# Kernel optimization log

Measured on AMD Instinct MI355X. Metric: run time of the kernel, lower is better.

The kernel has to match this reference:

```python
import jax, jax.numpy as jnp
import numpy as np

T, N, F, H, C, E = 8, 50000, 128, 64, 4, 800000


def setup_inputs() -> dict:
    key = jax.random.key(0)
    ks = jax.random.split(key, 8)
    x = jax.random.normal(ks[0], (T, N, F), jnp.float32)
    edges = jax.random.randint(ks[1], (T, 2, E), 0, N, jnp.int32)
    # GCNConv weights (one per timestep, glorot-ish scale) + Linear layers
    Wg = jax.random.normal(ks[2], (T, F, H), jnp.float32) / np.sqrt(F)
    bg = jnp.zeros((T, H), jnp.float32)
    W1 = jax.random.normal(ks[3], (H, 32), jnp.float32) / np.sqrt(H)
    b1 = jnp.zeros((32,), jnp.float32)
    W2 = jax.random.normal(ks[4], (32, 16), jnp.float32) / np.sqrt(32)
    b2 = jnp.zeros((16,), jnp.float32)
    W3 = jax.random.normal(ks[5], (16, C), jnp.float32) / np.sqrt(16)
    b3 = jnp.zeros((C,), jnp.float32)
    return dict(x=x, edges=edges, Wg=Wg, bg=bg, W1=W1, b1=b1, W2=W2, b2=b2, W3=W3, b3=b3)


def gcn_conv(x, edge_index, W, b):
    """PyG GCNConv: add self-loops, sym-normalized aggregation of x @ W, plus bias."""
    n = x.shape[0]
    loop = jnp.arange(n, dtype=edge_index.dtype)
    src = jnp.concatenate([edge_index[0], loop])  # message sources
    dst = jnp.concatenate([edge_index[1], loop])  # aggregation targets
    deg = jax.ops.segment_sum(jnp.ones_like(dst, dtype=x.dtype), dst, num_segments=n)
    dinv = jnp.where(deg > 0, jax.lax.rsqrt(deg), 0.0)
    xw = x @ W                                    # [n, H]
    norm = (dinv[src] * dinv[dst])[:, None]       # [E+n, 1]
    out = jax.ops.segment_sum(xw[src] * norm, dst, num_segments=n)
    return out + b


def reference(x, edges, Wg, bg, W1, b1, W2, b2, W3, b3):
    def step(acc, inp):
        xt, et, Wt, bt = inp
        return acc + jax.nn.relu(gcn_conv(xt, et, Wt, bt)), None

    acc0 = jnp.zeros((x.shape[1], Wg.shape[-1]), x.dtype)
    h, _ = jax.lax.scan(step, acc0, (x, edges, Wg, bg))  # sum over T timesteps
    h = jax.nn.relu(h)                 # dropout omitted (eval mode)
    h = jax.nn.relu(h @ W1 + b1)
    h = jax.nn.relu(h @ W2 + b2)
    logits = h @ W3 + b3
    return jax.nn.log_softmax(logits, axis=1)
```

## Files before the change

kernel.cpp:

```cpp
#include <hip/hip_runtime.h>
#include <hip/hip_bf16.h>

#define TT 8
#define NN 50000
#define FF 128
#define HH 64
#define CC 4
#define EE 800000
#define NB2 391
#define CAP 2560
#define BPT 125

typedef unsigned short u16;
typedef unsigned int u32;
typedef __attribute__((ext_vector_type(8))) short bf16x8;
typedef __attribute__((ext_vector_type(4))) float f32x4;
typedef __attribute__((ext_vector_type(4))) int i32x4;

static __device__ __forceinline__ float bflo(u32 w) {
    union { unsigned int i; float f; } v; v.i = w << 16; return v.f;
}
static __device__ __forceinline__ float bfhi(u32 w) {
    union { unsigned int i; float f; } v; v.i = w & 0xFFFF0000u; return v.f;
}
static __device__ __forceinline__ u16 cvt_bf16(float f) {
    __hip_bfloat16 b = __float2bfloat16(f);
    return *reinterpret_cast<u16*>(&b);
}

__global__ __launch_bounds__(256) void zero_gcur_kernel(int* __restrict__ gcur) {
    int i = blockIdx.x * 256 + threadIdx.x;
    if (i < TT * NB2) gcur[i] = 0;
}

__global__ __launch_bounds__(256) void multisplit_kernel(const int* __restrict__ edges,
                                                         int* __restrict__ gcur, u32* __restrict__ binned) {
    __shared__ u32 sbuf[NB2][16];
    __shared__ int scnt[NB2];
    int bid = blockIdx.x;
    int t = bid & 7;
    int blk = bid >> 3;
    const int per = EE / BPT;
    int e0 = blk * per;
    int e1 = e0 + per;

    for (int i = threadIdx.x; i < NB2; i += 256) scnt[i] = 0;
    __syncthreads();

    const int* es = edges + (size_t)(t * 2 + 0) * EE;
    const int* ed = edges + (size_t)(t * 2 + 1) * EE;
    int* gc = gcur + t * NB2;
    u32* bb = binned + (size_t)t * NB2 * CAP;

    for (int base = e0; base < e1; base += 1024) {
        u32 rec[4]; int pb[4];
        int e = base + threadIdx.x * 4;
        int nv = 0;
        if (e + 3 < e1) nv = 4;
        else if (e < e1) nv = e1 - e;
        if (nv == 4) {
            i32x4 s4 = *reinterpret_cast<const i32x4*>(&es[e]);
            i32x4 d4 = *reinterpret_cast<const i32x4*>(&ed[e]);
            #pragma unroll
            for (int q = 0; q < 4; ++q) {
                int b = d4[q] >> 7;
                u32 r = (u32)s4[q] | ((u32)(d4[q] & 127) << 16);
                int p = atomicAdd(&scnt[b], 1);
                if (p < 16) { sbuf[b][p] = r; pb[q] = -1; }
                else { rec[q] = r; pb[q] = b; }
            }
        } else {
            #pragma unroll
            for (int q = 0; q < 4; ++q) {
                pb[q] = -1;
                if (q < nv) {
                    int src = es[e + q], dst = ed[e + q];
                    int b = dst >> 7;
                    u32 r = (u32)src | ((u32)(dst & 127) << 16);
                    int p = atomicAdd(&scnt[b], 1);
                    if (p < 16) sbuf[b][p] = r;
                    else { rec[q] = r; pb[q] = b; }
                }
            }
        }
        __syncthreads();
        for (int fb = threadIdx.x; fb < NB2; fb += 256) {
            if (scnt[fb] >= 16) {
                int g = atomicAdd(&gc[fb], 16);
                uint4* dp = (uint4*)(bb + (size_t)fb * CAP + g);
                uint4* sp = (uint4*)&sbuf[fb][0];
                dp[0] = sp[0]; dp[1] = sp[1]; dp[2] = sp[2]; dp[3] = sp[3];
                scnt[fb] = 0;
            }
        }
        __syncthreads();
        #pragma unroll
        for (int q = 0; q < 4; ++q) {
            if (pb[q] >= 0) {
                int p = atomicAdd(&scnt[pb[q]], 1);
                if (p < 16) sbuf[pb[q]][p] = rec[q];
                else { int g = atomicAdd(&gc[pb[q]], 1); bb[(size_t)pb[q] * CAP + g] = rec[q]; }
            }
        }
        __syncthreads();
    }
    for (int fb = threadIdx.x; fb < NB2; fb += 256) {
        int c = scnt[fb];
        if (c > 0) {
            int g = atomicAdd(&gc[fb], c);
            for (int k = 0; k < c; ++k) bb[(size_t)fb * CAP + g + k] = sbuf[fb][k];
        }
    }
}

__global__ __launch_bounds__(512) void csr_scatter_kernel(const u32* __restrict__ binned, const int* __restrict__ gcur,
                                                          u16* __restrict__ srclist, u32* __restrict__ nodeinfo,
                                                          float* __restrict__ dinv) {
    __shared__ u32 recs[CAP];
    __shared__ int hist[128];
    __shared__ int cur[128];
    int b = blockIdx.x, t = blockIdx.y, tid = threadIdx.x;
    int node0 = b * 128;
    int tot = gcur[t * NB2 + b];
    const u32* win = binned + ((size_t)t * NB2 + b) * CAP;

    for (int i = tid; i < tot; i += 512) recs[i] = win[i];
    if (tid < 128) hist[tid] = 0;
    __syncthreads();
    for (int i = tid; i < tot; i += 512) atomicAdd(&hist[recs[i] >> 16], 1);
    __syncthreads();
    if (tid < 64) {
        int v0 = hist[2 * tid], v1 = hist[2 * tid + 1];
        int pair = v0 + v1;
        int inc = pair;
        #pragma unroll
        for (int off = 1; off < 64; off <<= 1) {
            int u = __shfl_up(inc, off, 64);
            if (tid >= off) inc += u;
        }
        int exclp = inc - pair;
        cur[2 * tid] = exclp;
        cur[2 * tid + 1] = exclp + v0;
        int node = node0 + 2 * tid;
        if (node < NN) {
            nodeinfo[t * NN + node] = (u32)(b * CAP + exclp) | ((u32)v0 << 20);
            dinv[t * NN + node] = rsqrtf(1.0f + (float)v0);
        }
        if (node + 1 < NN) {
            nodeinfo[t * NN + node + 1] = (u32)(b * CAP + exclp + v0) | ((u32)v1 << 20);
            dinv[t * NN + node + 1] = rsqrtf(1.0f + (float)v1);
        }
    }
    __syncthreads();
    u16* sl = srclist + (size_t)t * NB2 * CAP;
    for (int i = tid; i < tot; i += 512) {
        u32 rec = recs[i];
        int d = rec >> 16;
        int p = atomicAdd(&cur[d], 1);
        sl[(size_t)b * CAP + p] = (u16)(rec & 0xFFFF);
    }
}

__global__ __launch_bounds__(256) void wt_prep_kernel(const float* __restrict__ Wg, u16* __restrict__ wt) {
    int t = blockIdx.x;
    const float* w = Wg + t * FF * HH;
    u16* o = wt + (size_t)t * HH * FF;
    for (int i = threadIdx.x; i < FF * HH; i += 256) {
        int k = i >> 6, c = i & 63;
        o[c * FF + k] = cvt_bf16(w[i]);
    }
}

__global__ __launch_bounds__(512) void xw_kernel(const float* __restrict__ x, const u16* __restrict__ wt,
                                                 const float* __restrict__ dinv, u16* __restrict__ y) {
    int t = blockIdx.y;
    int row0 = blockIdx.x * 256;
    int tid = threadIdx.x;
    int w = tid >> 6, lane = tid & 63;
    int l15 = lane & 15, lg = lane >> 4;
    __shared__ __align__(16) u16 ylds[256][72];
    const float* xt = x + (size_t)t * NN * FF;
    const u16* wtt = wt + (size_t)t * HH * FF;

    f32x4 d[2][4] = {{{0,0,0,0},{0,0,0,0},{0,0,0,0},{0,0,0,0}},
                     {{0,0,0,0},{0,0,0,0},{0,0,0,0},{0,0,0,0}}};
    #pragma unroll
    for (int k0 = 0; k0 < 128; k0 += 32) {
        int kb = k0 + lg * 8;
        union { bf16x8 v; __hip_bfloat162 h[4]; } au[2];
        #pragma unroll
        for (int s = 0; s < 2; ++s) {
            int arow = row0 + w * 32 + s * 16 + l15;
            if (arow < NN) {
                f32x4 f0 = __builtin_nontemporal_load(reinterpret_cast<const f32x4*>(&xt[(size_t)arow * FF + kb]));
                f32x4 f1 = __builtin_nontemporal_load(reinterpret_cast<const f32x4*>(&xt[(size_t)arow * FF + kb + 4]));
                au[s].h[0] = __float22bfloat162_rn(make_float2(f0[0], f0[1]));
                au[s].h[1] = __float22bfloat162_rn(make_float2(f0[2], f0[3]));
                au[s].h[2] = __float22bfloat162_rn(make_float2(f1[0], f1[1]));
                au[s].h[3] = __float22bfloat162_rn(make_float2(f1[2], f1[3]));
            } else {
                au[s].v = (bf16x8){0,0,0,0,0,0,0,0};
            }
        }
        #pragma unroll
        for (int n = 0; n < 4; ++n) {
            bf16x8 bf = *reinterpret_cast<const bf16x8*>(&wtt[(size_t)(n * 16 + l15) * FF + kb]);
            d[0][n] = __builtin_amdgcn_mfma_f32_16x16x32_bf16(au[0].v, bf, d[0][n], 0, 0, 0);
            d[1][n] = __builtin_amdgcn_mfma_f32_16x16x32_bf16(au[1].v, bf, d[1][n], 0, 0, 0);
        }
    }
    #pragma unroll
    for (int s = 0; s < 2; ++s) {
        int rl = w * 32 + s * 16 + lg * 4;
        float dv[4];
        #pragma unroll
        for (int i = 0; i < 4; ++i) {
            int grow = row0 + rl + i;
            dv[i] = (grow < NN) ? dinv[t * NN + grow] : 0.f;
        }
        #pragma unroll
        for (int n = 0; n < 4; ++n) {
            int col = n * 16 + l15;
            #pragma unroll
            for (int i = 0; i < 4; ++i)
                ylds[rl + i][col] = cvt_bf16(d[s][n][i] * dv[i]);
        }
    }
    __syncthreads();
    u16* yt = y + (size_t)t * NN * HH;
    #pragma unroll
    for (int it = 0; it < 4; ++it) {
        int idx = it * 512 + tid;
        int r = idx >> 3, c8 = (idx & 7) * 8;
        int grow = row0 + r;
        if (grow < NN)
            *reinterpret_cast<uint4*>(&yt[(size_t)grow * HH + c8]) =
                *reinterpret_cast<const uint4*>(&ylds[r][c8]);
    }
}

__global__ __launch_bounds__(256) void agg_kernel(const u16* __restrict__ y, const float* __restrict__ dinv,
                                                  const u32* __restrict__ nodeinfo, const u16* __restrict__ srclist,
                                                  const float* __restrict__ bg, float* __restrict__ acc) {
    int node = blockIdx.x * 4 + (threadIdx.x >> 6);
    int lane = threadIdx.x & 63;
    int sub = lane >> 4;
    int fo = lane & 15;
    float a0 = 0.f, a1 = 0.f, a2 = 0.f, a3 = 0.f;
    for (int t = 0; t < TT; ++t) {
        const u16* yt = y + (size_t)t * NN * HH;
        u32 info = nodeinfo[t * NN + node];
        int cnt = info >> 20;
        const u16* sl = srclist + (size_t)t * NB2 * CAP + (info & 0xFFFFF);
        float s0 = 0.f, s1 = 0.f, s2 = 0.f, s3 = 0.f;
        int j = 0;
        for (; j + 16 <= cnt; j += 16) {
            int e0 = sl[j + sub], e1 = sl[j + 4 + sub], e2 = sl[j + 8 + sub], e3 = sl[j + 12 + sub];
            uint2 v0 = *reinterpret_cast<const uint2*>(&yt[(size_t)e0 * HH + fo * 4]);
            uint2 v1 = *reinterpret_cast<const uint2*>(&yt[(size_t)e1 * HH + fo * 4]);
            uint2 v2 = *reinterpret_cast<const uint2*>(&yt[(size_t)e2 * HH + fo * 4]);
            uint2 v3 = *reinterpret_cast<const uint2*>(&yt[(size_t)e3 * HH + fo * 4]);
            s0 += (bflo(v0.x) + bflo(v1.x)) + (bflo(v2.x) + bflo(v3.x));
            s1 += (bfhi(v0.x) + bfhi(v1.x)) + (bfhi(v2.x) + bfhi(v3.x));
            s2 += (bflo(v0.y) + bflo(v1.y)) + (bflo(v2.y) + bflo(v3.y));
            s3 += (bfhi(v0.y) + bfhi(v1.y)) + (bfhi(v2.y) + bfhi(v3.y));
        }
        for (; j < cnt; j += 4) {
            int e = j + sub;
            uint2 v = make_uint2(0u, 0u);
            if (e < cnt) {
                int srcid = sl[e];
                v = *reinterpret_cast<const uint2*>(&yt[(size_t)srcid * HH + fo * 4]);
            }
            s0 += bflo(v.x);
            s1 += bfhi(v.x);
            s2 += bflo(v.y);
            s3 += bfhi(v.y);
        }
        s0 += __shfl_xor(s0, 16, 64); s0 += __shfl_xor(s0, 32, 64);
        s1 += __shfl_xor(s1, 16, 64); s1 += __shfl_xor(s1, 32, 64);
        s2 += __shfl_xor(s2, 16, 64); s2 += __shfl_xor(s2, 32, 64);
        s3 += __shfl_xor(s3, 16, 64); s3 += __shfl_xor(s3, 32, 64);
        uint2 sv = *reinterpret_cast<const uint2*>(&yt[(size_t)node * HH + fo * 4]);
        s0 += bflo(sv.x);
        s1 += bfhi(sv.x);
        s2 += bflo(sv.y);
        s3 += bfhi(sv.y);
        float dvv = dinv[t * NN + node];
        float4 bgv = *reinterpret_cast<const float4*>(&bg[t * HH + fo * 4]);
        a0 += fmaxf(dvv * s0 + bgv.x, 0.f);
        a1 += fmaxf(dvv * s1 + bgv.y, 0.f);
        a2 += fmaxf(dvv * s2 + bgv.z, 0.f);
        a3 += fmaxf(dvv * s3 + bgv.w, 0.f);
    }
    if (sub == 0) {
        float4 o = make_float4(a0, a1, a2, a3);
        *reinterpret_cast<float4*>(&acc[(size_t)node * HH + fo * 4]) = o;
    }
}

__global__ __launch_bounds__(256) void head_kernel(const float* __restrict__ acc,
                                                   const float* __restrict__ W1, const float* __restrict__ b1,
                                                   const float* __restrict__ W2, const float* __restrict__ b2,
                                                   const float* __restrict__ W3, const float* __restrict__ b3,
                                                   float* __restrict__ out) {
    __shared__ float w1[64 * 32], w2[32 * 16], w3[16 * 4], bb1[32], bb2[16], bb3[4];
    int tid = threadIdx.x;
    for (int i = tid; i < 2048; i += 256) w1[i] = W1[i];
    for (int i = tid; i < 512; i += 256) w2[i] = W2[i];
    if (tid < 64) w3[tid] = W3[tid];
    if (tid < 32) bb1[tid] = b1[tid];
    if (tid < 16) bb2[tid] = b2[tid];
    if (tid < 4) bb3[tid] = b3[tid];
    __syncthreads();
    int node = blockIdx.x * 256 + tid;
    if (node >= NN) return;

    float a[64];
    #pragma unroll
    for (int k = 0; k < 64; ++k) a[k] = acc[(size_t)node * HH + k];

    float h1[32];
    for (int j = 0; j < 32; ++j) {
        float s = bb1[j];
        #pragma unroll
        for (int k = 0; k < 64; ++k) s += a[k] * w1[k * 32 + j];
        h1[j] = fmaxf(s, 0.f);
    }
    float h2[16];
    for (int j = 0; j < 16; ++j) {
        float s = bb2[j];
        #pragma unroll
        for (int k = 0; k < 32; ++k) s += h1[k] * w2[k * 16 + j];
        h2[j] = fmaxf(s, 0.f);
    }
    float l[4];
    for (int c = 0; c < 4; ++c) {
        float s = bb3[c];
        #pragma unroll
        for (int k = 0; k < 16; ++k) s += h2[k] * w3[k * 4 + c];
        l[c] = s;
    }
    float m = fmaxf(fmaxf(l[0], l[1]), fmaxf(l[2], l[3]));
    float sum = 0.f;
    #pragma unroll
    for (int c = 0; c < 4; ++c) sum += expf(l[c] - m);
    float lse = logf(sum);
    float4 o;
    o.x = l[0] - m - lse; o.y = l[1] - m - lse; o.z = l[2] - m - lse; o.w = l[3] - m - lse;
    *reinterpret_cast<float4*>(&out[(size_t)node * CC]) = o;
}

extern "C" void kernel_launch(void* const* d_in, const int* in_sizes, int n_in,
                              void* d_out, int out_size, void* d_ws, size_t ws_size,
                              hipStream_t stream) {
    const float* x    = (const float*)d_in[0];
    const int*  edges = (const int*)d_in[1];
    const float* Wg   = (const float*)d_in[2];
    const float* bg   = (const float*)d_in[3];
    const float* W1   = (const float*)d_in[4];
    const float* b1   = (const float*)d_in[5];
    const float* W2   = (const float*)d_in[6];
    const float* b2   = (const float*)d_in[7];
    const float* W3   = (const float*)d_in[8];
    const float* b3   = (const float*)d_in[9];
    float* out = (float*)d_out;

    char* ws = (char*)d_ws;
    size_t o = 0;
    int* gcur      = (int*)(ws + o); o += (size_t)TT * NB2 * 4;
    o = (o + 255) & ~(size_t)255;
    float* dinv    = (float*)(ws + o); o += (size_t)TT * NN * 4;
    u32* nodeinfo  = (u32*)(ws + o); o += (size_t)TT * NN * 4;
    o = (o + 255) & ~(size_t)255;
    u16* wt        = (u16*)(ws + o); o += (size_t)TT * HH * FF * 2;
    o = (o + 255) & ~(size_t)255;
    u32* binned    = (u32*)(ws + o); o += (size_t)TT * NB2 * CAP * 4;
    u16* srclist   = (u16*)(ws + o); o += (size_t)TT * NB2 * CAP * 2;
    u16* y         = (u16*)(ws + o); o += (size_t)TT * NN * HH * 2;
    float* acc     = (float*)(ws + o); o += (size_t)NN * HH * 4;

    zero_gcur_kernel<<<(TT * NB2 + 255) / 256, 256, 0, stream>>>(gcur);

    multisplit_kernel<<<BPT * TT, 256, 0, stream>>>(edges, gcur, binned);

    dim3 gsc(NB2, TT);
    csr_scatter_kernel<<<gsc, 512, 0, stream>>>(binned, gcur, srclist, nodeinfo, dinv);

    wt_prep_kernel<<<TT, 256, 0, stream>>>(Wg, wt);

    dim3 gx(196, TT);
    xw_kernel<<<gx, 512, 0, stream>>>(x, wt, dinv, y);

    agg_kernel<<<12500, 256, 0, stream>>>(y, dinv, nodeinfo, srclist, bg, acc);

    head_kernel<<<196, 256, 0, stream>>>(acc, W1, b1, W2, b2, W3, b3, out);
}
```

Before: 338.3 us.

## Count degrees in multisplit and co-schedule CSR build with XW GEMM

Per-node in-degree is now counted with global atomics during the edge multisplit pass. This lets the CSR scatter and the x@W GEMM run as interleaved block roles of a single launch, instead of the GEMM waiting on a separate CSR kernel for dinv. The dinv array is dropped: each consumer recomputes it from the degree counts with rsqrt. The aggregation loop is also unrolled to 32 edges per iteration to keep more gathers in flight. In exchange, it adds 6.4M global atomics on a zeroed 1.6MB count array and a larger zeroing kernel.

```diff
diff --git a/kernel.cpp b/kernel.cpp
--- a/kernel.cpp
+++ b/kernel.cpp
@@ -10,6 +10,7 @@
 #define NB2 391
 #define CAP 2560
 #define BPT 125
+#define XWB 196
 
 typedef unsigned short u16;
 typedef unsigned int u32;
@@ -28,13 +29,15 @@
     return *reinterpret_cast<u16*>(&b);
 }
 
-__global__ __launch_bounds__(256) void zero_gcur_kernel(int* __restrict__ gcur) {
+__global__ __launch_bounds__(256) void zero_kernel(int* __restrict__ cnt, int* __restrict__ gcur) {
     int i = blockIdx.x * 256 + threadIdx.x;
-    if (i < TT * NB2) gcur[i] = 0;
+    if (i < TT * NN) cnt[i] = 0;
+    else if (i < TT * NN + TT * NB2) gcur[i - TT * NN] = 0;
 }
 
 __global__ __launch_bounds__(256) void multisplit_kernel(const int* __restrict__ edges,
-                                                         int* __restrict__ gcur, u32* __restrict__ binned) {
+                                                         int* __restrict__ gcur, u32* __restrict__ binned,
+                                                         int* __restrict__ cnt) {
     __shared__ u32 sbuf[NB2][16];
     __shared__ int scnt[NB2];
     int bid = blockIdx.x;
@@ -50,6 +53,7 @@
     const int* es = edges + (size_t)(t * 2 + 0) * EE;
     const int* ed = edges + (size_t)(t * 2 + 1) * EE;
     int* gc = gcur + t * NB2;
+    int* cw = cnt + t * NN;
     u32* bb = binned + (size_t)t * NB2 * CAP;
 
     for (int base = e0; base < e1; base += 1024) {
@@ -65,6 +69,7 @@
             for (int q = 0; q < 4; ++q) {
                 int b = d4[q] >> 7;
                 u32 r = (u32)s4[q] | ((u32)(d4[q] & 127) << 16);
+                atomicAdd(&cw[d4[q]], 1);
                 int p = atomicAdd(&scnt[b], 1);
                 if (p < 16) { sbuf[b][p] = r; pb[q] = -1; }
                 else { rec[q] = r; pb[q] = b; }
@@ -77,6 +82,7 @@
                     int src = es[e + q], dst = ed[e + q];
                     int b = dst >> 7;
                     u32 r = (u32)src | ((u32)(dst & 127) << 16);
+                    atomicAdd(&cw[dst], 1);
                     int p = atomicAdd(&scnt[b], 1);
                     if (p < 16) sbuf[b][p] = r;
                     else { rec[q] = r; pb[q] = b; }
@@ -113,54 +119,6 @@
     }
 }
 
-__global__ __launch_bounds__(512) void csr_scatter_kernel(const u32* __restrict__ binned, const int* __restrict__ gcur,
-                                                          u16* __restrict__ srclist, u32* __restrict__ nodeinfo,
-                                                          float* __restrict__ dinv) {
-    __shared__ u32 recs[CAP];
-    __shared__ int hist[128];
-    __shared__ int cur[128];
-    int b = blockIdx.x, t = blockIdx.y, tid = threadIdx.x;
-    int node0 = b * 128;
-    int tot = gcur[t * NB2 + b];
-    const u32* win = binned + ((size_t)t * NB2 + b) * CAP;
-
-    for (int i = tid; i < tot; i += 512) recs[i] = win[i];
-    if (tid < 128) hist[tid] = 0;
-    __syncthreads();
-    for (int i = tid; i < tot; i += 512) atomicAdd(&hist[recs[i] >> 16], 1);
-    __syncthreads();
-    if (tid < 64) {
-        int v0 = hist[2 * tid], v1 = hist[2 * tid + 1];
-        int pair = v0 + v1;
-        int inc = pair;
-        #pragma unroll
-        for (int off = 1; off < 64; off <<= 1) {
-            int u = __shfl_up(inc, off, 64);
-            if (tid >= off) inc += u;
-        }
-        int exclp = inc - pair;
-        cur[2 * tid] = exclp;
-        cur[2 * tid + 1] = exclp + v0;
-        int node = node0 + 2 * tid;
-        if (node < NN) {
-            nodeinfo[t * NN + node] = (u32)(b * CAP + exclp) | ((u32)v0 << 20);
-            dinv[t * NN + node] = rsqrtf(1.0f + (float)v0);
-        }
-        if (node + 1 < NN) {
-            nodeinfo[t * NN + node + 1] = (u32)(b * CAP + exclp + v0) | ((u32)v1 << 20);
-            dinv[t * NN + node + 1] = rsqrtf(1.0f + (float)v1);
-        }
-    }
-    __syncthreads();
-    u16* sl = srclist + (size_t)t * NB2 * CAP;
-    for (int i = tid; i < tot; i += 512) {
-        u32 rec = recs[i];
-        int d = rec >> 16;
-        int p = atomicAdd(&cur[d], 1);
-        sl[(size_t)b * CAP + p] = (u16)(rec & 0xFFFF);
-    }
-}
-
 __global__ __launch_bounds__(256) void wt_prep_kernel(const float* __restrict__ Wg, u16* __restrict__ wt) {
     int t = blockIdx.x;
     const float* w = Wg + t * FF * HH;
@@ -171,75 +129,124 @@
     }
 }
 
-__global__ __launch_bounds__(512) void xw_kernel(const float* __restrict__ x, const u16* __restrict__ wt,
-                                                 const float* __restrict__ dinv, u16* __restrict__ y) {
-    int t = blockIdx.y;
-    int row0 = blockIdx.x * 256;
+__global__ __launch_bounds__(512) void build_kernel(const u32* __restrict__ binned, const int* __restrict__ gcur,
+                                                    const int* __restrict__ cnt,
+                                                    u16* __restrict__ srclist, u32* __restrict__ nodeinfo,
+                                                    const float* __restrict__ x, const u16* __restrict__ wt,
+                                                    u16* __restrict__ y) {
+    __shared__ __align__(16) char smem[256 * 72 * 2];
+    int bid = blockIdx.x;
     int tid = threadIdx.x;
-    int w = tid >> 6, lane = tid & 63;
-    int l15 = lane & 15, lg = lane >> 4;
-    __shared__ __align__(16) u16 ylds[256][72];
-    const float* xt = x + (size_t)t * NN * FF;
-    const u16* wtt = wt + (size_t)t * HH * FF;
-
-    f32x4 d[2][4] = {{{0,0,0,0},{0,0,0,0},{0,0,0,0},{0,0,0,0}},
-                     {{0,0,0,0},{0,0,0,0},{0,0,0,0},{0,0,0,0}}};
-    #pragma unroll
-    for (int k0 = 0; k0 < 128; k0 += 32) {
-        int kb = k0 + lg * 8;
-        union { bf16x8 v; __hip_bfloat162 h[4]; } au[2];
+    int isXw, id;
+    if (bid < 2 * XWB * TT) { isXw = ((bid & 1) == 0); id = bid >> 1; }
+    else { isXw = 0; id = XWB * TT + (bid - 2 * XWB * TT); }
+
+    if (!isXw) {
+        u32* recs = (u32*)smem;
+        int* cur = (int*)(smem + CAP * 4);
+        int t = id / NB2, b = id % NB2;
+        int node0 = b * 128;
+        int tot = gcur[t * NB2 + b];
+        const u32* win = binned + ((size_t)t * NB2 + b) * CAP;
+        const int* cw = cnt + t * NN;
+        for (int i = tid; i < tot; i += 512) recs[i] = win[i];
+        __syncthreads();
+        if (tid < 64) {
+            int n0 = node0 + 2 * tid;
+            int v0 = (n0 < NN) ? cw[n0] : 0;
+            int v1 = (n0 + 1 < NN) ? cw[n0 + 1] : 0;
+            int pair = v0 + v1;
+            int inc = pair;
+            #pragma unroll
+            for (int off = 1; off < 64; off <<= 1) {
+                int u = __shfl_up(inc, off, 64);
+                if (tid >= off) inc += u;
+            }
+            int exclp = inc - pair;
+            cur[2 * tid] = exclp;
+            cur[2 * tid + 1] = exclp + v0;
+            if (n0 < NN)
+                nodeinfo[t * NN + n0] = (u32)(b * CAP + exclp) | ((u32)v0 << 20);
+            if (n0 + 1 < NN)
+                nodeinfo[t * NN + n0 + 1] = (u32)(b * CAP + exclp + v0) | ((u32)v1 << 20);
+        }
+        __syncthreads();
+        u16* sl = srclist + (size_t)t * NB2 * CAP;
+        for (int i = tid; i < tot; i += 512) {
+            u32 rec = recs[i];
+            int d = rec >> 16;
+            int p = atomicAdd(&cur[d], 1);
+            sl[(size_t)b * CAP + p] = (u16)(rec & 0xFFFF);
+        }
+    } else {
+        u16 (*ylds)[72] = (u16(*)[72])smem;
+        int t = id / XWB, xb = id % XWB;
+        int row0 = xb * 256;
+        int w = tid >> 6, lane = tid & 63;
+        int l15 = lane & 15, lg = lane >> 4;
+        const float* xt = x + (size_t)t * NN * FF;
+        const u16* wtt = wt + (size_t)t * HH * FF;
+        const int* cw = cnt + t * NN;
+
+        f32x4 d[2][4] = {{{0,0,0,0},{0,0,0,0},{0,0,0,0},{0,0,0,0}},
+                         {{0,0,0,0},{0,0,0,0},{0,0,0,0},{0,0,0,0}}};
+        #pragma unroll
+        for (int k0 = 0; k0 < 128; k0 += 32) {
+            int kb = k0 + lg * 8;
+            union { bf16x8 v; __hip_bfloat162 h[4]; } au[2];
+            #pragma unroll
+            for (int s = 0; s < 2; ++s) {
+                int arow = row0 + w * 32 + s * 16 + l15;
+                if (arow < NN) {
+                    f32x4 f0 = __builtin_nontemporal_load(reinterpret_cast<const f32x4*>(&xt[(size_t)arow * FF + kb]));
+                    f32x4 f1 = __builtin_nontemporal_load(reinterpret_cast<const f32x4*>(&xt[(size_t)arow * FF + kb + 4]));
+                    au[s].h[0] = __float22bfloat162_rn(make_float2(f0[0], f0[1]));
+                    au[s].h[1] = __float22bfloat162_rn(make_float2(f0[2], f0[3]));
+                    au[s].h[2] = __float22bfloat162_rn(make_float2(f1[0], f1[1]));
+                    au[s].h[3] = __float22bfloat162_rn(make_float2(f1[2], f1[3]));
+                } else {
+                    au[s].v = (bf16x8){0,0,0,0,0,0,0,0};
+                }
+            }
+            #pragma unroll
+            for (int n = 0; n < 4; ++n) {
+                bf16x8 bf = *reinterpret_cast<const bf16x8*>(&wtt[(size_t)(n * 16 + l15) * FF + kb]);
+                d[0][n] = __builtin_amdgcn_mfma_f32_16x16x32_bf16(au[0].v, bf, d[0][n], 0, 0, 0);
+                d[1][n] = __builtin_amdgcn_mfma_f32_16x16x32_bf16(au[1].v, bf, d[1][n], 0, 0, 0);
+            }
+        }
         #pragma unroll
         for (int s = 0; s < 2; ++s) {
-            int arow = row0 + w * 32 + s * 16 + l15;
-            if (arow < NN) {
-                f32x4 f0 = __builtin_nontemporal_load(reinterpret_cast<const f32x4*>(&xt[(size_t)arow * FF + kb]));
-                f32x4 f1 = __builtin_nontemporal_load(reinterpret_cast<const f32x4*>(&xt[(size_t)arow * FF + kb + 4]));
-                au[s].h[0] = __float22bfloat162_rn(make_float2(f0[0], f0[1]));
-                au[s].h[1] = __float22bfloat162_rn(make_float2(f0[2], f0[3]));
-                au[s].h[2] = __float22bfloat162_rn(make_float2(f1[0], f1[1]));
-                au[s].h[3] = __float22bfloat162_rn(make_float2(f1[2], f1[3]));
-            } else {
-                au[s].v = (bf16x8){0,0,0,0,0,0,0,0};
-            }
-        }
-        #pragma unroll
-        for (int n = 0; n < 4; ++n) {
-            bf16x8 bf = *reinterpret_cast<const bf16x8*>(&wtt[(size_t)(n * 16 + l15) * FF + kb]);
-            d[0][n] = __builtin_amdgcn_mfma_f32_16x16x32_bf16(au[0].v, bf, d[0][n], 0, 0, 0);
-            d[1][n] = __builtin_amdgcn_mfma_f32_16x16x32_bf16(au[1].v, bf, d[1][n], 0, 0, 0);
-        }
-    }
-    #pragma unroll
-    for (int s = 0; s < 2; ++s) {
-        int rl = w * 32 + s * 16 + lg * 4;
-        float dv[4];
-        #pragma unroll
-        for (int i = 0; i < 4; ++i) {
-            int grow = row0 + rl + i;
-            dv[i] = (grow < NN) ? dinv[t * NN + grow] : 0.f;
-        }
-        #pragma unroll
-        for (int n = 0; n < 4; ++n) {
-            int col = n * 16 + l15;
-            #pragma unroll
-            for (int i = 0; i < 4; ++i)
-                ylds[rl + i][col] = cvt_bf16(d[s][n][i] * dv[i]);
-        }
-    }
-    __syncthreads();
-    u16* yt = y + (size_t)t * NN * HH;
-    #pragma unroll
-    for (int it = 0; it < 4; ++it) {
-        int idx = it * 512 + tid;
-        int r = idx >> 3, c8 = (idx & 7) * 8;
-        int grow = row0 + r;
-        if (grow < NN)
-            *reinterpret_cast<uint4*>(&yt[(size_t)grow * HH + c8]) =
-                *reinterpret_cast<const uint4*>(&ylds[r][c8]);
-    }
-}
-
-__global__ __launch_bounds__(256) void agg_kernel(const u16* __restrict__ y, const float* __restrict__ dinv,
+            int rl = w * 32 + s * 16 + lg * 4;
+            float dv[4];
+            #pragma unroll
+            for (int i = 0; i < 4; ++i) {
+                int grow = row0 + rl + i;
+                dv[i] = (grow < NN) ? rsqrtf(1.f + (float)cw[grow]) : 0.f;
+            }
+            #pragma unroll
+            for (int n = 0; n < 4; ++n) {
+                int col = n * 16 + l15;
+                #pragma unroll
+                for (int i = 0; i < 4; ++i)
+                    ylds[rl + i][col] = cvt_bf16(d[s][n][i] * dv[i]);
+            }
+        }
+        __syncthreads();
+        u16* yt = y + (size_t)t * NN * HH;
+        #pragma unroll
+        for (int it = 0; it < 4; ++it) {
+            int idx = it * 512 + tid;
+            int r = idx >> 3, c8 = (idx & 7) * 8;
+            int grow = row0 + r;
+            if (grow < NN)
+                *reinterpret_cast<uint4*>(&yt[(size_t)grow * HH + c8]) =
+                    *reinterpret_cast<const uint4*>(&ylds[r][c8]);
+        }
+    }
+}
+
+__global__ __launch_bounds__(256) void agg_kernel(const u16* __restrict__ y,
                                                   const u32* __restrict__ nodeinfo, const u16* __restrict__ srclist,
                                                   const float* __restrict__ bg, float* __restrict__ acc) {
     int node = blockIdx.x * 4 + (threadIdx.x >> 6);
@@ -254,7 +261,27 @@
         const u16* sl = srclist + (size_t)t * NB2 * CAP + (info & 0xFFFFF);
         float s0 = 0.f, s1 = 0.f, s2 = 0.f, s3 = 0.f;
         int j = 0;
-        for (; j + 16 <= cnt; j += 16) {
+        for (; j + 32 <= cnt; j += 32) {
+            int e0 = sl[j + sub],      e1 = sl[j + 4 + sub],  e2 = sl[j + 8 + sub],  e3 = sl[j + 12 + sub];
+            int e4 = sl[j + 16 + sub], e5 = sl[j + 20 + sub], e6 = sl[j + 24 + sub], e7 = sl[j + 28 + sub];
+            uint2 v0 = *reinterpret_cast<const uint2*>(&yt[(size_t)e0 * HH + fo * 4]);
+            uint2 v1 = *reinterpret_cast<const uint2*>(&yt[(size_t)e1 * HH + fo * 4]);
+            uint2 v2 = *reinterpret_cast<const uint2*>(&yt[(size_t)e2 * HH + fo * 4]);
+            uint2 v3 = *reinterpret_cast<const uint2*>(&yt[(size_t)e3 * HH + fo * 4]);
+            uint2 v4 = *reinterpret_cast<const uint2*>(&yt[(size_t)e4 * HH + fo * 4]);
+            uint2 v5 = *reinterpret_cast<const uint2*>(&yt[(size_t)e5 * HH + fo * 4]);
+            uint2 v6 = *reinterpret_cast<const uint2*>(&yt[(size_t)e6 * HH + fo * 4]);
+            uint2 v7 = *reinterpret_cast<const uint2*>(&yt[(size_t)e7 * HH + fo * 4]);
+            s0 += ((bflo(v0.x) + bflo(v1.x)) + (bflo(v2.x) + bflo(v3.x)))
+                + ((bflo(v4.x) + bflo(v5.x)) + (bflo(v6.x) + bflo(v7.x)));
+            s1 += ((bfhi(v0.x) + bfhi(v1.x)) + (bfhi(v2.x) + bfhi(v3.x)))
+                + ((bfhi(v4.x) + bfhi(v5.x)) + (bfhi(v6.x) + bfhi(v7.x)));
+            s2 += ((bflo(v0.y) + bflo(v1.y)) + (bflo(v2.y) + bflo(v3.y)))
+                + ((bflo(v4.y) + bflo(v5.y)) + (bflo(v6.y) + bflo(v7.y)));
+            s3 += ((bfhi(v0.y) + bfhi(v1.y)) + (bfhi(v2.y) + bfhi(v3.y)))
+                + ((bfhi(v4.y) + bfhi(v5.y)) + (bfhi(v6.y) + bfhi(v7.y)));
+        }
+        if (j + 16 <= cnt) {
             int e0 = sl[j + sub], e1 = sl[j + 4 + sub], e2 = sl[j + 8 + sub], e3 = sl[j + 12 + sub];
             uint2 v0 = *reinterpret_cast<const uint2*>(&yt[(size_t)e0 * HH + fo * 4]);
             uint2 v1 = *reinterpret_cast<const uint2*>(&yt[(size_t)e1 * HH + fo * 4]);
@@ -264,6 +291,7 @@
             s1 += (bfhi(v0.x) + bfhi(v1.x)) + (bfhi(v2.x) + bfhi(v3.x));
             s2 += (bflo(v0.y) + bflo(v1.y)) + (bflo(v2.y) + bflo(v3.y));
             s3 += (bfhi(v0.y) + bfhi(v1.y)) + (bfhi(v2.y) + bfhi(v3.y));
+            j += 16;
         }
         for (; j < cnt; j += 4) {
             int e = j + sub;
@@ -286,7 +314,7 @@
         s1 += bfhi(sv.x);
         s2 += bflo(sv.y);
         s3 += bfhi(sv.y);
-        float dvv = dinv[t * NN + node];
+        float dvv = rsqrtf(1.f + (float)cnt);
         float4 bgv = *reinterpret_cast<const float4*>(&bg[t * HH + fo * 4]);
         a0 += fmaxf(dvv * s0 + bgv.x, 0.f);
         a1 += fmaxf(dvv * s1 + bgv.y, 0.f);
@@ -370,7 +398,7 @@
     size_t o = 0;
     int* gcur      = (int*)(ws + o); o += (size_t)TT * NB2 * 4;
     o = (o + 255) & ~(size_t)255;
-    float* dinv    = (float*)(ws + o); o += (size_t)TT * NN * 4;
+    int* cnt       = (int*)(ws + o); o += (size_t)TT * NN * 4;
     u32* nodeinfo  = (u32*)(ws + o); o += (size_t)TT * NN * 4;
     o = (o + 255) & ~(size_t)255;
     u16* wt        = (u16*)(ws + o); o += (size_t)TT * HH * FF * 2;
@@ -380,19 +408,16 @@
     u16* y         = (u16*)(ws + o); o += (size_t)TT * NN * HH * 2;
     float* acc     = (float*)(ws + o); o += (size_t)NN * HH * 4;
 
-    zero_gcur_kernel<<<(TT * NB2 + 255) / 256, 256, 0, stream>>>(gcur);
-
-    multisplit_kernel<<<BPT * TT, 256, 0, stream>>>(edges, gcur, binned);
-
-    dim3 gsc(NB2, TT);
-    csr_scatter_kernel<<<gsc, 512, 0, stream>>>(binned, gcur, srclist, nodeinfo, dinv);
+    zero_kernel<<<(TT * NN + TT * NB2 + 255) / 256, 256, 0, stream>>>(cnt, gcur);
 
     wt_prep_kernel<<<TT, 256, 0, stream>>>(Wg, wt);
 
-    dim3 gx(196, TT);
-    xw_kernel<<<gx, 512, 0, stream>>>(x, wt, dinv, y);
-
-    agg_kernel<<<12500, 256, 0, stream>>>(y, dinv, nodeinfo, srclist, bg, acc);
+    multisplit_kernel<<<BPT * TT, 256, 0, stream>>>(edges, gcur, binned, cnt);
+
+    build_kernel<<<XWB * TT + NB2 * TT, 512, 0, stream>>>(binned, gcur, cnt, srclist, nodeinfo,
+                                                          x, wt, y);
+
+    agg_kernel<<<12500, 256, 0, stream>>>(y, nodeinfo, srclist, bg, acc);
 
     head_kernel<<<196, 256, 0, stream>>>(acc, W1, b1, W2, b2, W3, b3, out);
 }
```

After: 583.7 us. 72.5% more time.

## Merge edge multisplit and XW GEMM into one interleaved kernel

Applied to the files above, without the earlier changes.

Fuses the edge-binning multisplit and the dense X·W bf16 MFMA GEMM into a single launch whose blocks are interleaved, one multisplit block per three GEMM blocks, so the atomic-heavy binning overlaps the bandwidth-bound GEMM. The dinv source scaling moves out of the GEMM epilogue into csr_scatter, which rescales y in place per bucket. The dinv buffer goes away because agg recomputes rsqrt from the count. The cost is an extra read-modify-write pass over y, a second bf16 rounding of y, and GEMM blocks shrunk to 128 rows and 256 threads.

```diff
diff --git a/kernel.cpp b/kernel.cpp
--- a/kernel.cpp
+++ b/kernel.cpp
@@ -10,6 +10,7 @@
 #define NB2 391
 #define CAP 2560
 #define BPT 125
+#define XWB 391
 
 typedef unsigned short u16;
 typedef unsigned int u32;
@@ -33,89 +34,171 @@
     if (i < TT * NB2) gcur[i] = 0;
 }
 
-__global__ __launch_bounds__(256) void multisplit_kernel(const int* __restrict__ edges,
-                                                         int* __restrict__ gcur, u32* __restrict__ binned) {
-    __shared__ u32 sbuf[NB2][16];
-    __shared__ int scnt[NB2];
+__global__ __launch_bounds__(256) void wt_prep_kernel(const float* __restrict__ Wg, u16* __restrict__ wt) {
+    int t = blockIdx.x;
+    const float* w = Wg + t * FF * HH;
+    u16* o = wt + (size_t)t * HH * FF;
+    for (int i = threadIdx.x; i < FF * HH; i += 256) {
+        int k = i >> 6, c = i & 63;
+        o[c * FF + k] = cvt_bf16(w[i]);
+    }
+}
+
+__global__ __launch_bounds__(256) void ms_xw_kernel(const int* __restrict__ edges,
+                                                    int* __restrict__ gcur, u32* __restrict__ binned,
+                                                    const float* __restrict__ x, const u16* __restrict__ wt,
+                                                    u16* __restrict__ y) {
+    __shared__ __align__(16) char smem[26624];
     int bid = blockIdx.x;
-    int t = bid & 7;
-    int blk = bid >> 3;
-    const int per = EE / BPT;
-    int e0 = blk * per;
-    int e1 = e0 + per;
-
-    for (int i = threadIdx.x; i < NB2; i += 256) scnt[i] = 0;
-    __syncthreads();
-
-    const int* es = edges + (size_t)(t * 2 + 0) * EE;
-    const int* ed = edges + (size_t)(t * 2 + 1) * EE;
-    int* gc = gcur + t * NB2;
-    u32* bb = binned + (size_t)t * NB2 * CAP;
-
-    for (int base = e0; base < e1; base += 1024) {
-        u32 rec[4]; int pb[4];
-        int e = base + threadIdx.x * 4;
-        int nv = 0;
-        if (e + 3 < e1) nv = 4;
-        else if (e < e1) nv = e1 - e;
-        if (nv == 4) {
-            i32x4 s4 = *reinterpret_cast<const i32x4*>(&es[e]);
-            i32x4 d4 = *reinterpret_cast<const i32x4*>(&ed[e]);
+    int tid = threadIdx.x;
+    int isMs, id;
+    if (bid < 4 * BPT * TT) {
+        isMs = ((bid & 3) == 0);
+        id = isMs ? (bid >> 2) : ((bid >> 2) * 3 + (bid & 3) - 1);
+    } else {
+        isMs = 0; id = 3 * BPT * TT + (bid - 4 * BPT * TT);
+    }
+
+    if (isMs) {
+        u32 (*sbuf)[16] = (u32(*)[16])smem;
+        int* scnt = (int*)(smem + NB2 * 16 * 4);
+        int t = id & 7;
+        int blk = id >> 3;
+        const int per = EE / BPT;
+        int e0 = blk * per;
+        int e1 = e0 + per;
+
+        for (int i = tid; i < NB2; i += 256) scnt[i] = 0;
+        __syncthreads();
+
+        const int* es = edges + (size_t)(t * 2 + 0) * EE;
+        const int* ed = edges + (size_t)(t * 2 + 1) * EE;
+        int* gc = gcur + t * NB2;
+        u32* bb = binned + (size_t)t * NB2 * CAP;
+
+        for (int base = e0; base < e1; base += 1024) {
+            u32 rec[4]; int pb[4];
+            int e = base + tid * 4;
+            int nv = 0;
+            if (e + 3 < e1) nv = 4;
+            else if (e < e1) nv = e1 - e;
+            if (nv == 4) {
+                i32x4 s4 = *reinterpret_cast<const i32x4*>(&es[e]);
+                i32x4 d4 = *reinterpret_cast<const i32x4*>(&ed[e]);
+                #pragma unroll
+                for (int q = 0; q < 4; ++q) {
+                    int b = d4[q] >> 7;
+                    u32 r = (u32)s4[q] | ((u32)(d4[q] & 127) << 16);
+                    int p = atomicAdd(&scnt[b], 1);
+                    if (p < 16) { sbuf[b][p] = r; pb[q] = -1; }
+                    else { rec[q] = r; pb[q] = b; }
+                }
+            } else {
+                #pragma unroll
+                for (int q = 0; q < 4; ++q) {
+                    pb[q] = -1;
+                    if (q < nv) {
+                        int src = es[e + q], dst = ed[e + q];
+                        int b = dst >> 7;
+                        u32 r = (u32)src | ((u32)(dst & 127) << 16);
+                        int p = atomicAdd(&scnt[b], 1);
+                        if (p < 16) sbuf[b][p] = r;
+                        else { rec[q] = r; pb[q] = b; }
+                    }
+                }
+            }
+            __syncthreads();
+            for (int fb = tid; fb < NB2; fb += 256) {
+                if (scnt[fb] >= 16) {
+                    int g = atomicAdd(&gc[fb], 16);
+                    uint4* dp = (uint4*)(bb + (size_t)fb * CAP + g);
+                    uint4* sp = (uint4*)&sbuf[fb][0];
+                    dp[0] = sp[0]; dp[1] = sp[1]; dp[2] = sp[2]; dp[3] = sp[3];
+                    scnt[fb] = 0;
+                }
+            }
+            __syncthreads();
             #pragma unroll
             for (int q = 0; q < 4; ++q) {
-                int b = d4[q] >> 7;
-                u32 r = (u32)s4[q] | ((u32)(d4[q] & 127) << 16);
-                int p = atomicAdd(&scnt[b], 1);
-                if (p < 16) { sbuf[b][p] = r; pb[q] = -1; }
-                else { rec[q] = r; pb[q] = b; }
-            }
-        } else {
+                if (pb[q] >= 0) {
+                    int p = atomicAdd(&scnt[pb[q]], 1);
+                    if (p < 16) sbuf[pb[q]][p] = rec[q];
+                    else { int g = atomicAdd(&gc[pb[q]], 1); bb[(size_t)pb[q] * CAP + g] = rec[q]; }
+                }
+            }
+            __syncthreads();
+        }
+        for (int fb = tid; fb < NB2; fb += 256) {
+            int c = scnt[fb];
+            if (c > 0) {
+                int g = atomicAdd(&gc[fb], c);
+                for (int k = 0; k < c; ++k) bb[(size_t)fb * CAP + g + k] = sbuf[fb][k];
+            }
+        }
+    } else {
+        u16 (*ylds)[72] = (u16(*)[72])smem;
+        int t = id / XWB, xb = id % XWB;
+        int row0 = xb * 128;
+        int w = tid >> 6, lane = tid & 63;
+        int l15 = lane & 15, lg = lane >> 4;
+        const float* xt = x + (size_t)t * NN * FF;
+        const u16* wtt = wt + (size_t)t * HH * FF;
+
+        f32x4 d[2][4] = {{{0,0,0,0},{0,0,0,0},{0,0,0,0},{0,0,0,0}},
+                         {{0,0,0,0},{0,0,0,0},{0,0,0,0},{0,0,0,0}}};
+        #pragma unroll
+        for (int k0 = 0; k0 < 128; k0 += 32) {
+            int kb = k0 + lg * 8;
+            union { bf16x8 v; __hip_bfloat162 h[4]; } au[2];
             #pragma unroll
-            for (int q = 0; q < 4; ++q) {
-                pb[q] = -1;
-                if (q < nv) {
-                    int src = es[e + q], dst = ed[e + q];
-                    int b = dst >> 7;
-                    u32 r = (u32)src | ((u32)(dst & 127) << 16);
-                    int p = atomicAdd(&scnt[b], 1);
-                    if (p < 16) sbuf[b][p] = r;
-                    else { rec[q] = r; pb[q] = b; }
+            for (int s = 0; s < 2; ++s) {
+                int arow = row0 + w * 32 + s * 16 + l15;
+                if (arow < NN) {
+                    f32x4 f0 = __builtin_nontemporal_load(reinterpret_cast<const f32x4*>(&xt[(size_t)arow * FF + kb]));
+                    f32x4 f1 = __builtin_nontemporal_load(reinterpret_cast<const f32x4*>(&xt[(size_t)arow * FF + kb + 4]));
+                    au[s].h[0] = __float22bfloat162_rn(make_float2(f0[0], f0[1]));
+                    au[s].h[1] = __float22bfloat162_rn(make_float2(f0[2], f0[3]));
+                    au[s].h[2] = __float22bfloat162_rn(make_float2(f1[0], f1[1]));
+                    au[s].h[3] = __float22bfloat162_rn(make_float2(f1[2], f1[3]));
+                } else {
+                    au[s].v = (bf16x8){0,0,0,0,0,0,0,0};
                 }
             }
+            #pragma unroll
+            for (int n = 0; n < 4; ++n) {
+                bf16x8 bf = *reinterpret_cast<const bf16x8*>(&wtt[(size_t)(n * 16 + l15) * FF + kb]);
+                d[0][n] = __builtin_amdgcn_mfma_f32_16x16x32_bf16(au[0].v, bf, d[0][n], 0, 0, 0);
+                d[1][n] = __builtin_amdgcn_mfma_f32_16x16x32_bf16(au[1].v, bf, d[1][n], 0, 0, 0);
+            }
+        }
+        #pragma unroll
+        for (int s = 0; s < 2; ++s) {
+            int rl = w * 32 + s * 16 + lg * 4;
+            #pragma unroll
+            for (int n = 0; n < 4; ++n) {
+                int col = n * 16 + l15;
+                #pragma unroll
+                for (int i = 0; i < 4; ++i)
+                    ylds[rl + i][col] = cvt_bf16(d[s][n][i]);
+            }
         }
         __syncthreads();
-        for (int fb = threadIdx.x; fb < NB2; fb += 256) {
-            if (scnt[fb] >= 16) {
-                int g = atomicAdd(&gc[fb], 16);
-                uint4* dp = (uint4*)(bb + (size_t)fb * CAP + g);
-                uint4* sp = (uint4*)&sbuf[fb][0];
-                dp[0] = sp[0]; dp[1] = sp[1]; dp[2] = sp[2]; dp[3] = sp[3];
-                scnt[fb] = 0;
-            }
-        }
-        __syncthreads();
-        #pragma unroll
-        for (int q = 0; q < 4; ++q) {
-            if (pb[q] >= 0) {
-                int p = atomicAdd(&scnt[pb[q]], 1);
-                if (p < 16) sbuf[pb[q]][p] = rec[q];
-                else { int g = atomicAdd(&gc[pb[q]], 1); bb[(size_t)pb[q] * CAP + g] = rec[q]; }
-            }
-        }
-        __syncthreads();
-    }
-    for (int fb = threadIdx.x; fb < NB2; fb += 256) {
-        int c = scnt[fb];
-        if (c > 0) {
-            int g = atomicAdd(&gc[fb], c);
-            for (int k = 0; k < c; ++k) bb[(size_t)fb * CAP + g + k] = sbuf[fb][k];
+        u16* yt = y + (size_t)t * NN * HH;
+        #pragma unroll
+        for (int it = 0; it < 4; ++it) {
+            int idx = it * 256 + tid;
+            int r = idx >> 3, c8 = (idx & 7) * 8;
+            int grow = row0 + r;
+            if (grow < NN)
+                *reinterpret_cast<uint4*>(&yt[(size_t)grow * HH + c8]) =
+                    *reinterpret_cast<const uint4*>(&ylds[r][c8]);
         }
     }
 }
 
 __global__ __launch_bounds__(512) void csr_scatter_kernel(const u32* __restrict__ binned, const int* __restrict__ gcur,
                                                           u16* __restrict__ srclist, u32* __restrict__ nodeinfo,
-                                                          float* __restrict__ dinv) {
+                                                          u16* __restrict__ y) {
     __shared__ u32 recs[CAP];
     __shared__ int hist[128];
     __shared__ int cur[128];
@@ -142,14 +225,10 @@
         cur[2 * tid] = exclp;
         cur[2 * tid + 1] = exclp + v0;
         int node = node0 + 2 * tid;
-        if (node < NN) {
+        if (node < NN)
             nodeinfo[t * NN + node] = (u32)(b * CAP + exclp) | ((u32)v0 << 20);
-            dinv[t * NN + node] = rsqrtf(1.0f + (float)v0);
-        }
-        if (node + 1 < NN) {
+        if (node + 1 < NN)
             nodeinfo[t * NN + node + 1] = (u32)(b * CAP + exclp + v0) | ((u32)v1 << 20);
-            dinv[t * NN + node + 1] = rsqrtf(1.0f + (float)v1);
-        }
     }
     __syncthreads();
     u16* sl = srclist + (size_t)t * NB2 * CAP;
@@ -159,87 +238,27 @@
         int p = atomicAdd(&cur[d], 1);
         sl[(size_t)b * CAP + p] = (u16)(rec & 0xFFFF);
     }
-}
-
-__global__ __launch_bounds__(256) void wt_prep_kernel(const float* __restrict__ Wg, u16* __restrict__ wt) {
-    int t = blockIdx.x;
-    const float* w = Wg + t * FF * HH;
-    u16* o = wt + (size_t)t * HH * FF;
-    for (int i = threadIdx.x; i < FF * HH; i += 256) {
-        int k = i >> 6, c = i & 63;
-        o[c * FF + k] = cvt_bf16(w[i]);
-    }
-}
-
-__global__ __launch_bounds__(512) void xw_kernel(const float* __restrict__ x, const u16* __restrict__ wt,
-                                                 const float* __restrict__ dinv, u16* __restrict__ y) {
-    int t = blockIdx.y;
-    int row0 = blockIdx.x * 256;
-    int tid = threadIdx.x;
-    int w = tid >> 6, lane = tid & 63;
-    int l15 = lane & 15, lg = lane >> 4;
-    __shared__ __align__(16) u16 ylds[256][72];
-    const float* xt = x + (size_t)t * NN * FF;
-    const u16* wtt = wt + (size_t)t * HH * FF;
-
-    f32x4 d[2][4] = {{{0,0,0,0},{0,0,0,0},{0,0,0,0},{0,0,0,0}},
-                     {{0,0,0,0},{0,0,0,0},{0,0,0,0},{0,0,0,0}}};
-    #pragma unroll
-    for (int k0 = 0; k0 < 128; k0 += 32) {
-        int kb = k0 + lg * 8;
-        union { bf16x8 v; __hip_bfloat162 h[4]; } au[2];
-        #pragma unroll
-        for (int s = 0; s < 2; ++s) {
-            int arow = row0 + w * 32 + s * 16 + l15;
-            if (arow < NN) {
-                f32x4 f0 = __builtin_nontemporal_load(reinterpret_cast<const f32x4*>(&xt[(size_t)arow * FF + kb]));
-                f32x4 f1 = __builtin_nontemporal_load(reinterpret_cast<const f32x4*>(&xt[(size_t)arow * FF + kb + 4]));
-                au[s].h[0] = __float22bfloat162_rn(make_float2(f0[0], f0[1]));
-                au[s].h[1] = __float22bfloat162_rn(make_float2(f0[2], f0[3]));
-                au[s].h[2] = __float22bfloat162_rn(make_float2(f1[0], f1[1]));
-                au[s].h[3] = __float22bfloat162_rn(make_float2(f1[2], f1[3]));
-            } else {
-                au[s].v = (bf16x8){0,0,0,0,0,0,0,0};
-            }
-        }
-        #pragma unroll
-        for (int n = 0; n < 4; ++n) {
-            bf16x8 bf = *reinterpret_cast<const bf16x8*>(&wtt[(size_t)(n * 16 + l15) * FF + kb]);
-            d[0][n] = __builtin_amdgcn_mfma_f32_16x16x32_bf16(au[0].v, bf, d[0][n], 0, 0, 0);
-            d[1][n] = __builtin_amdgcn_mfma_f32_16x16x32_bf16(au[1].v, bf, d[1][n], 0, 0, 0);
-        }
-    }
-    #pragma unroll
-    for (int s = 0; s < 2; ++s) {
-        int rl = w * 32 + s * 16 + lg * 4;
-        float dv[4];
-        #pragma unroll
-        for (int i = 0; i < 4; ++i) {
-            int grow = row0 + rl + i;
-            dv[i] = (grow < NN) ? dinv[t * NN + grow] : 0.f;
-        }
-        #pragma unroll
-        for (int n = 0; n < 4; ++n) {
-            int col = n * 16 + l15;
+    u16* yt = y + (size_t)t * NN * HH;
+    for (int idx = tid; idx < 128 * 8; idx += 512) {
+        int r = idx >> 3, c8 = (idx & 7) * 8;
+        int grow = node0 + r;
+        if (grow < NN) {
+            float dv = rsqrtf(1.f + (float)hist[r]);
+            uint4* p = reinterpret_cast<uint4*>(&yt[(size_t)grow * HH + c8]);
+            uint4 v = *p;
+            u32 ww[4] = {v.x, v.y, v.z, v.w};
             #pragma unroll
-            for (int i = 0; i < 4; ++i)
-                ylds[rl + i][col] = cvt_bf16(d[s][n][i] * dv[i]);
-        }
-    }
-    __syncthreads();
-    u16* yt = y + (size_t)t * NN * HH;
-    #pragma unroll
-    for (int it = 0; it < 4; ++it) {
-        int idx = it * 512 + tid;
-        int r = idx >> 3, c8 = (idx & 7) * 8;
-        int grow = row0 + r;
-        if (grow < NN)
-            *reinterpret_cast<uint4*>(&yt[(size_t)grow * HH + c8]) =
-                *reinterpret_cast<const uint4*>(&ylds[r][c8]);
-    }
-}
-
-__global__ __launch_bounds__(256) void agg_kernel(const u16* __restrict__ y, const float* __restrict__ dinv,
+            for (int k = 0; k < 4; ++k) {
+                float lo = bflo(ww[k]) * dv;
+                float hi = bfhi(ww[k]) * dv;
+                ww[k] = (u32)cvt_bf16(lo) | ((u32)cvt_bf16(hi) << 16);
+            }
+            *p = make_uint4(ww[0], ww[1], ww[2], ww[3]);
+        }
+    }
+}
+
+__global__ __launch_bounds__(256) void agg_kernel(const u16* __restrict__ y,
                                                   const u32* __restrict__ nodeinfo, const u16* __restrict__ srclist,
                                                   const float* __restrict__ bg, float* __restrict__ acc) {
     int node = blockIdx.x * 4 + (threadIdx.x >> 6);
@@ -286,7 +305,7 @@
         s1 += bfhi(sv.x);
         s2 += bflo(sv.y);
         s3 += bfhi(sv.y);
-        float dvv = dinv[t * NN + node];
+        float dvv = rsqrtf(1.f + (float)cnt);
         float4 bgv = *reinterpret_cast<const float4*>(&bg[t * HH + fo * 4]);
         a0 += fmaxf(dvv * s0 + bgv.x, 0.f);
         a1 += fmaxf(dvv * s1 + bgv.y, 0.f);
@@ -370,7 +389,6 @@
     size_t o = 0;
     int* gcur      = (int*)(ws + o); o += (size_t)TT * NB2 * 4;
     o = (o + 255) & ~(size_t)255;
-    float* dinv    = (float*)(ws + o); o += (size_t)TT * NN * 4;
     u32* nodeinfo  = (u32*)(ws + o); o += (size_t)TT * NN * 4;
     o = (o + 255) & ~(size_t)255;
     u16* wt        = (u16*)(ws + o); o += (size_t)TT * HH * FF * 2;
@@ -382,17 +400,15 @@
 
     zero_gcur_kernel<<<(TT * NB2 + 255) / 256, 256, 0, stream>>>(gcur);
 
-    multisplit_kernel<<<BPT * TT, 256, 0, stream>>>(edges, gcur, binned);
+    wt_prep_kernel<<<TT, 256, 0, stream>>>(Wg, wt);
+
+    ms_xw_kernel<<<4 * BPT * TT + (XWB * TT - 3 * BPT * TT), 256, 0, stream>>>(
+        edges, gcur, binned, x, wt, y);
 
     dim3 gsc(NB2, TT);
-    csr_scatter_kernel<<<gsc, 512, 0, stream>>>(binned, gcur, srclist, nodeinfo, dinv);
-
-    wt_prep_kernel<<<TT, 256, 0, stream>>>(Wg, wt);
-
-    dim3 gx(196, TT);
-    xw_kernel<<<gx, 512, 0, stream>>>(x, wt, dinv, y);
-
-    agg_kernel<<<12500, 256, 0, stream>>>(y, dinv, nodeinfo, srclist, bg, acc);
+    csr_scatter_kernel<<<gsc, 512, 0, stream>>>(binned, gcur, srclist, nodeinfo, y);
+
+    agg_kernel<<<12500, 256, 0, stream>>>(y, nodeinfo, srclist, bg, acc);
 
     head_kernel<<<196, 256, 0, stream>>>(acc, W1, b1, W2, b2, W3, b3, out);
 }
```

After: 322.5 us. -4.7%, faster.
